# Performance work log

Measured on AMD Instinct MI355X. Metric: run time of the kernel, lower is better.

## Reference

```python
import jax, jax.numpy as jnp
import numpy as np

# Loihi neuron / simulation constants (params['neuron'], params['simulation'])
VTH_MANT = 80
V_DECAY = 128
I_DECAY = 1024
REF_DELAY = 1
WGT_EXP = 0
TAU_RHO = 1.0
SCALE_RHO = 1.0
TS = 1
THETA = float(VTH_MANT * (1 << 6))      # 5120, Loihi threshold in fixed-point units
W_SCALE = float(1 << (6 + WGT_EXP))     # 64, weight scaling into Loihi fixed point


def st_floor(x):
    """floor with straight-through gradient (Loihi integer truncation)."""
    return x + jax.lax.stop_gradient(jnp.floor(x) - x)


@jax.custom_vjp
def spike_fn(v):
    # binary spike scaled by 1/Ts, as in SLAYER-Loihi
    return (v >= THETA).astype(v.dtype) * (1.0 / TS)

def _spike_fwd(v):
    return spike_fn(v), v

def _spike_bwd(v, g):
    # SLAYER surrogate: scaleRho/(tauRho*theta) * exp(-|v - theta| / (tauRho*theta))
    pdf = (SCALE_RHO / (TAU_RHO * THETA)) * jnp.exp(-jnp.abs(v - THETA) / (TAU_RHO * THETA))
    return (g * pdf,)

spike_fn.defvjp(_spike_fwd, _spike_bwd)


def quantize_w(w, step=2.0):
    """SLAYER snn.utils.quantize(w, 2) with straight-through gradient."""
    return w + jax.lax.stop_gradient(jnp.round(w / step) * step - w)


def loihi_spikes(wsp):
    """Loihi CUBA neuron scan. wsp: [T, B, C] weighted spike input -> [T, B, C] spikes."""
    i_mul = (4096.0 - I_DECAY) / 4096.0
    v_mul = (4096.0 - V_DECAY) / 4096.0

    def step(carry, x):
        I, V, ref = carry
        I = st_floor(I * i_mul) + W_SCALE * x
        V = st_floor(V * v_mul) + I
        V = jnp.where(ref > 0, jnp.zeros_like(V), V)   # refractory hold at 0
        s = spike_fn(V)
        V = V * (1.0 - s * TS)                          # reset to 0 on spike
        ref = jnp.where(s > 0, REF_DELAY - 1, jnp.maximum(ref - 1, 0))
        return (I, V, ref), s

    B, C = wsp.shape[1], wsp.shape[2]
    init = (jnp.zeros((B, C), wsp.dtype),
            jnp.zeros((B, C), wsp.dtype),
            jnp.zeros((B, C), jnp.int32))
    _, s = jax.lax.scan(step, init, wsp)
    return s


def delay_shift(x):
    """delayShift(x, 1): shift spikes one step forward in time. x: [T, B, C]."""
    return jnp.concatenate([jnp.zeros_like(x[:1]), x[:-1]], axis=0)


def setup_inputs() -> dict:
    key = jax.random.key(0)
    k1, k2, k3 = jax.random.split(key, 3)
    B, IN, HID, OUT, T = 32, 1024, 2048, 512, 256
    spike_input = (jax.random.uniform(k1, (B, IN, T)) < 0.05).astype(jnp.float32)
    W1 = jax.random.normal(k2, (HID, IN), jnp.float32) * 8.0
    W2 = jax.random.normal(k3, (OUT, HID), jnp.float32) * 8.0
    return {"spike_input": spike_input, "W1": W1, "W2": W2}


def reference(spike_input, W1, W2):
    # spike_input: [B, IN, T] binary spikes
    x = jnp.transpose(spike_input, (2, 0, 1))          # [T, B, IN]
    w1 = quantize_w(W1)
    w2 = quantize_w(W2)
    h = jnp.einsum('tbi,hi->tbh', x, w1)               # fc1 per timestep
    s1 = delay_shift(loihi_spikes(h))                  # spikeLoihi + delayShift(1)
    o = jnp.einsum('tbh,oh->tbo', s1, w2)              # fc2 per timestep
    s2 = delay_shift(loihi_spikes(o))
    return jnp.transpose(s2, (1, 2, 0))                # [B, OUT, T]
```

## Files before the change

### kernel.cpp

```cpp
#include <hip/hip_runtime.h>

typedef unsigned char u8;
typedef signed char i8;
typedef unsigned int u32;
typedef __attribute__((ext_vector_type(4))) int i32x4;

#define AS1 __attribute__((address_space(1)))
#define AS3 __attribute__((address_space(3)))

__device__ __forceinline__ void gload_lds16(const void* g, void* l) {
    __builtin_amdgcn_global_load_lds((const AS1 void*)g, (AS3 void*)l, 16, 0, 0);
}

__global__ void transpose_x_bt(const float* __restrict__ X, i8* __restrict__ Xb,
                               int B, int IN, int T) {
    __shared__ float tile[128][33];
    const int t0 = blockIdx.x * 32, i0 = blockIdx.y * 128, b = blockIdx.z;
    const int tx = threadIdx.x & 31, ty = threadIdx.x >> 5;
    const float* src = X + (size_t)b * IN * T;
#pragma unroll
    for (int r = 0; r < 16; ++r) {
        int i = ty + r * 8;
        tile[i][tx] = src[(size_t)(i0 + i) * T + t0 + tx];
    }
    __syncthreads();
    const int cx = threadIdx.x & 31;
    const int tl0 = threadIdx.x >> 5;
#pragma unroll
    for (int r = 0; r < 4; ++r) {
        int tl = tl0 + r * 8;
        uchar4 pk;
        pk.x = (tile[cx * 4 + 0][tl] != 0.f) ? 1 : 0;
        pk.y = (tile[cx * 4 + 1][tl] != 0.f) ? 1 : 0;
        pk.z = (tile[cx * 4 + 2][tl] != 0.f) ? 1 : 0;
        pk.w = (tile[cx * 4 + 3][tl] != 0.f) ? 1 : 0;
        *(uchar4*)&Xb[((size_t)b * T + t0 + tl) * IN + i0 + cx * 4] = pk;
    }
}

__global__ void quant_both(const float4* __restrict__ W1, const float4* __restrict__ W2,
                           char4* __restrict__ W1q, char4* __restrict__ W2q,
                           int n1v, int n2v) {
    int i = blockIdx.x * 256 + threadIdx.x;
    if (i < n1v) {
        float4 w = W1[i];
        char4 q;
        q.x = (i8)(int)rintf(w.x * 0.5f);
        q.y = (i8)(int)rintf(w.y * 0.5f);
        q.z = (i8)(int)rintf(w.z * 0.5f);
        q.w = (i8)(int)rintf(w.w * 0.5f);
        W1q[i] = q;
    } else if (i < n1v + n2v) {
        int j = i - n1v;
        float4 w = W2[j];
        char4 q;
        q.x = (i8)(int)rintf(w.x * 0.5f);
        q.y = (i8)(int)rintf(w.y * 0.5f);
        q.z = (i8)(int)rintf(w.z * 0.5f);
        q.w = (i8)(int)rintf(w.w * 0.5f);
        W2q[j] = q;
    }
}

__global__ __launch_bounds__(256, 4) void gemm1_scan1(
        const i8* __restrict__ A, const i8* __restrict__ Bt,
        i8* __restrict__ S1, int K) {
    __shared__ __align__(16) i8 lds[40960];
    i8*    lA   = lds;
    i8*    lB   = lds + 32768;
    short* hT   = (short*)lds;
    u32*   bits = (u32*)(lds + 32768);

    const int nwg = gridDim.x;
    const int cpx = nwg >> 3;
    const int wg  = (blockIdx.x & 7) * cpx + (blockIdx.x >> 3);
    const int scanw = (blockIdx.x >> 3) & 3;
    const int bx = wg & 31;
    const int by = wg >> 5;
    const int n0 = bx * 64;
    const int m0 = by * 256;

    const int tid  = threadIdx.x;
    const int lane = tid & 63;
    const int w    = tid >> 6;
    const int l15 = lane & 15;
    const int l4  = lane >> 4;
    const int sw  = l15 & 7;

    i32x4 acc[4][4] = {};
    const int flatT = tid * 16;

    for (int k0 = 0; k0 < K; k0 += 128) {
        __syncthreads();
#pragma unroll
        for (int q = 0; q < 8; ++q) {
            int fl = q * 4096 + flatT;
            int r  = fl >> 7;
            int sc = ((fl >> 4) & 7) ^ (r & 7);
            gload_lds16(A + (size_t)(m0 + r) * K + k0 + sc * 16, &lA[fl]);
        }
#pragma unroll
        for (int q = 0; q < 2; ++q) {
            int fl = q * 4096 + flatT;
            int r  = fl >> 7;
            int sc = ((fl >> 4) & 7) ^ (r & 7);
            gload_lds16(Bt + (size_t)(n0 + r) * K + k0 + sc * 16, &lB[fl]);
        }
        __syncthreads();
#pragma unroll
        for (int kk = 0; kk < 2; ++kk) {
            i32x4 af[4], bf[4];
#pragma unroll
            for (int mf = 0; mf < 4; ++mf)
                af[mf] = *(const i32x4*)&lA[(w * 64 + mf * 16 + l15) * 128 +
                                            ((kk * 4 + l4) ^ sw) * 16];
#pragma unroll
            for (int nf = 0; nf < 4; ++nf)
                bf[nf] = *(const i32x4*)&lB[(nf * 16 + l15) * 128 +
                                            ((kk * 4 + l4) ^ sw) * 16];
#pragma unroll
            for (int mf = 0; mf < 4; ++mf)
#pragma unroll
                for (int nf = 0; nf < 4; ++nf)
                    acc[mf][nf] = __builtin_amdgcn_mfma_i32_16x16x64_i8(
                        af[mf], bf[nf], acc[mf][nf], 0, 0, 0);
        }
    }
    __syncthreads();

#pragma unroll
    for (int mf = 0; mf < 4; ++mf)
#pragma unroll
        for (int nf = 0; nf < 4; ++nf) {
            int n = nf * 16 + l15;
            int c = w * 16 + mf * 4 + l4;
            int h0 = acc[mf][nf][0] * 2, h1 = acc[mf][nf][1] * 2;
            int h2 = acc[mf][nf][2] * 2, h3 = acc[mf][nf][3] * 2;
            int2 pk;
            pk.x = (h0 & 0xffff) | (h1 << 16);
            pk.y = (h2 & 0xffff) | (h3 << 16);
            *(int2*)((char*)hT + n * 512 + ((c ^ (n & 15)) << 3)) = pk;
        }
    __syncthreads();

    if (w == scanw) {
        const int n = lane;
        const int nx = n & 15;
        const char* hrow = (char*)hT + n * 512;
        int2 ra[4], rb[4];
#pragma unroll
        for (int q = 0; q < 4; ++q)
            ra[q] = *(const int2*)(hrow + ((q ^ nx) << 3));
        u32 bw[8] = {0, 0, 0, 0, 0, 0, 0, 0};
        float I = 0.f, V = 0.f;
#pragma unroll
        for (int p = 0; p < 16; ++p) {
            if (p < 15) {
#pragma unroll
                for (int q = 0; q < 4; ++q) {
                    int2 v = *(const int2*)(hrow + ((((p + 1) * 4 + q) ^ nx) << 3));
                    if (p & 1) ra[q] = v; else rb[q] = v;
                }
            }
#pragma unroll
            for (int q = 0; q < 4; ++q) {
                int2 hh = (p & 1) ? rb[q] : ra[q];
#pragma unroll
                for (int j = 0; j < 4; ++j) {
                    int t = p * 16 + q * 4 + j;
                    short hv = (j == 0) ? (short)hh.x
                             : (j == 1) ? (short)(hh.x >> 16)
                             : (j == 2) ? (short)hh.y
                                        : (short)(hh.y >> 16);
                    I = floorf(I * 0.75f) + 64.f * (float)hv;
                    V = floorf(V * 0.96875f) + I;
                    if (V >= 5120.f) { bw[t >> 5] |= (1u << (t & 31)); V = 0.f; }
                }
            }
        }
#pragma unroll
        for (int wi = 0; wi < 8; ++wi) bits[wi * 64 + n] = bw[wi];
    }
    __syncthreads();

#pragma unroll
    for (int rep = 0; rep < 16; ++rep) {
        int d   = rep * 256 + tid;
        int tt  = d >> 4;
        int ndq = d & 15;
        u32 outw = 0;
        if (tt > 0) {
            int tb = tt - 1, wi = tb >> 5, sh = tb & 31;
            outw =  ((bits[wi * 64 + ndq * 4 + 0] >> sh) & 1)
                 | (((bits[wi * 64 + ndq * 4 + 1] >> sh) & 1) << 8)
                 | (((bits[wi * 64 + ndq * 4 + 2] >> sh) & 1) << 16)
                 | (((bits[wi * 64 + ndq * 4 + 3] >> sh) & 1) << 24);
        }
        *(u32*)&S1[(size_t)(m0 + tt) * 2048 + n0 + ndq * 4] = outw;
    }
}

__global__ __launch_bounds__(256, 1) void gemm2_scan2(
        const i8* __restrict__ A, const i8* __restrict__ Bt,
        float* __restrict__ out, int K) {
    __shared__ __align__(16) i8 lds[67584];
    i8*    lA   = lds;
    i8*    lB   = lds + 32768;
    float* hT   = (float*)lds;
    u32*   bits = (u32*)(lds + 65536);

    const int nwg = gridDim.x;
    const int cpx = nwg >> 3;
    const int wg  = (blockIdx.x & 7) * cpx + (blockIdx.x >> 3);
    const int scanw = (blockIdx.x >> 3) & 3;
    const int ox = wg & 7;
    const int by = wg >> 3;
    const int n0 = ox * 64;
    const int m0 = by * 256;

    const int tid  = threadIdx.x;
    const int lane = tid & 63;
    const int w    = tid >> 6;
    const int l15 = lane & 15;
    const int l4  = lane >> 4;
    const int sw  = l15 & 7;

    i32x4 acc[4][4] = {};
    const int flatT = tid * 16;

    for (int k0 = 0; k0 < K; k0 += 128) {
        __syncthreads();
#pragma unroll
        for (int q = 0; q < 8; ++q) {
            int fl = q * 4096 + flatT;
            int r  = fl >> 7;
            int sc = ((fl >> 4) & 7) ^ (r & 7);
            gload_lds16(A + (size_t)(m0 + r) * K + k0 + sc * 16, &lA[fl]);
        }
#pragma unroll
        for (int q = 0; q < 2; ++q) {
            int fl = q * 4096 + flatT;
            int r  = fl >> 7;
            int sc = ((fl >> 4) & 7) ^ (r & 7);
            gload_lds16(Bt + (size_t)(n0 + r) * K + k0 + sc * 16, &lB[fl]);
        }
        __syncthreads();
#pragma unroll
        for (int kk = 0; kk < 2; ++kk) {
            i32x4 af[4], bf[4];
#pragma unroll
            for (int mf = 0; mf < 4; ++mf)
                af[mf] = *(const i32x4*)&lA[(w * 64 + mf * 16 + l15) * 128 +
                                            ((kk * 4 + l4) ^ sw) * 16];
#pragma unroll
            for (int nf = 0; nf < 4; ++nf)
                bf[nf] = *(const i32x4*)&lB[(nf * 16 + l15) * 128 +
                                            ((kk * 4 + l4) ^ sw) * 16];
#pragma unroll
            for (int mf = 0; mf < 4; ++mf)
#pragma unroll
                for (int nf = 0; nf < 4; ++nf)
                    acc[mf][nf] = __builtin_amdgcn_mfma_i32_16x16x64_i8(
                        af[mf], bf[nf], acc[mf][nf], 0, 0, 0);
        }
    }
    __syncthreads();

#pragma unroll
    for (int mf = 0; mf < 4; ++mf)
#pragma unroll
        for (int nf = 0; nf < 4; ++nf) {
            int n = nf * 16 + l15;
            int c = w * 16 + mf * 4 + l4;
            float4 pk;
            pk.x = (float)(acc[mf][nf][0] * 2);
            pk.y = (float)(acc[mf][nf][1] * 2);
            pk.z = (float)(acc[mf][nf][2] * 2);
            pk.w = (float)(acc[mf][nf][3] * 2);
            *(float4*)((char*)hT + n * 1024 + ((c ^ (n & 15)) << 4)) = pk;
        }
    __syncthreads();

    if (w == scanw) {
        const int n = lane;
        const int nx = n & 15;
        const char* hrow = (char*)hT + n * 1024;
        float4 ra[4], rb[4];
#pragma unroll
        for (int q = 0; q < 4; ++q)
            ra[q] = *(const float4*)(hrow + ((q ^ nx) << 4));
        u32 bw[8] = {0, 0, 0, 0, 0, 0, 0, 0};
        float I = 0.f, V = 0.f;
#pragma unroll
        for (int p = 0; p < 16; ++p) {
            if (p < 15) {
#pragma unroll
                for (int q = 0; q < 4; ++q) {
                    float4 v = *(const float4*)(hrow + ((((p + 1) * 4 + q) ^ nx) << 4));
                    if (p & 1) ra[q] = v; else rb[q] = v;
                }
            }
#pragma unroll
            for (int q = 0; q < 4; ++q) {
                float4 hh = (p & 1) ? rb[q] : ra[q];
#pragma unroll
                for (int j = 0; j < 4; ++j) {
                    int t = p * 16 + q * 4 + j;
                    float hv = (j == 0) ? hh.x : (j == 1) ? hh.y
                             : (j == 2) ? hh.z : hh.w;
                    I = floorf(I * 0.75f) + 64.f * hv;
                    V = floorf(V * 0.96875f) + I;
                    if (V >= 5120.f) { bw[t >> 5] |= (1u << (t & 31)); V = 0.f; }
                }
            }
        }
#pragma unroll
        for (int wi = 0; wi < 8; ++wi) bits[wi * 64 + n] = bw[wi];
    }
    __syncthreads();

#pragma unroll
    for (int rep = 0; rep < 16; ++rep) {
        int flat = rep * 256 + tid;
        int o  = flat >> 6;
        int t4 = flat & 63;
        float4 v;
#pragma unroll
        for (int j = 0; j < 4; ++j) {
            int tt = t4 * 4 + j;
            float s = 0.f;
            if (tt > 0) {
                int tb = tt - 1;
                s = (float)((bits[(tb >> 5) * 64 + o] >> (tb & 31)) & 1);
            }
            if (j == 0) v.x = s; else if (j == 1) v.y = s;
            else if (j == 2) v.z = s; else v.w = s;
        }
        *(float4*)&out[((size_t)by * 512 + n0 + o) * 256 + t4 * 4] = v;
    }
}

extern "C" void kernel_launch(void* const* d_in, const int* in_sizes, int n_in,
                              void* d_out, int out_size, void* d_ws, size_t ws_size,
                              hipStream_t stream) {
    const int B = 32, IN = 1024, HID = 2048, OUT = 512, T = 256;
    const float* spikes = (const float*)d_in[0];
    const float* W1 = (const float*)d_in[1];
    const float* W2 = (const float*)d_in[2];
    float* out = (float*)d_out;

    char* ws = (char*)d_ws;
    size_t off = 0;
    auto alloc = [&](size_t bytes) -> void* {
        void* p = ws + off;
        off += (bytes + 255) & ~(size_t)255;
        return p;
    };
    i8* Xb  = (i8*)alloc((size_t)B * T * IN);
    i8* W1q = (i8*)alloc((size_t)HID * IN);
    i8* W2q = (i8*)alloc((size_t)OUT * HID);
    i8* S1  = (i8*)alloc((size_t)B * T * HID);

    dim3 blk(256);
    transpose_x_bt<<<dim3(T / 32, IN / 128, B), blk, 0, stream>>>(spikes, Xb, B, IN, T);
    {
        int n1v = HID * IN / 4, n2v = OUT * HID / 4;
        quant_both<<<dim3((n1v + n2v + 255) / 256), blk, 0, stream>>>(
            (const float4*)W1, (const float4*)W2, (char4*)W1q, (char4*)W2q, n1v, n2v);
    }
    gemm1_scan1<<<dim3(1024), blk, 0, stream>>>(Xb, W1q, S1, IN);
    gemm2_scan2<<<dim3(256), blk, 0, stream>>>(S1, W2q, out, HID);
}
```

Baseline: 75.47 us.

## Use 1024-thread blocks with double-buffered LDS pipeline in gemm2_scan2

gemm2_scan2 now runs 16 waves per workgroup instead of 4. Each wave owns a 16-row slice of the 256-row M tile rather than 64 rows. The K loop is double-buffered: the next 128-wide K tile is staged into the alternate LDS buffer while MFMA runs on the current one, leaving one barrier per iteration. The goal is more latency hiding and overlap of loads with compute, at the cost of higher LDS use (84 KB), less register reuse of B fragments per wave, and a serial per-block scan that now sits beside more idle waves.

```diff
diff --git a/kernel.cpp b/kernel.cpp
--- a/kernel.cpp
+++ b/kernel.cpp
@@ -200,19 +200,17 @@
     }
 }
 
-__global__ __launch_bounds__(256, 1) void gemm2_scan2(
+__global__ __launch_bounds__(1024, 1) void gemm2_scan2(
         const i8* __restrict__ A, const i8* __restrict__ Bt,
         float* __restrict__ out, int K) {
-    __shared__ __align__(16) i8 lds[67584];
-    i8*    lA   = lds;
-    i8*    lB   = lds + 32768;
+    __shared__ __align__(16) i8 lds[83968];
     float* hT   = (float*)lds;
-    u32*   bits = (u32*)(lds + 65536);
+    u32*   bits = (u32*)(lds + 81920);
 
     const int nwg = gridDim.x;
     const int cpx = nwg >> 3;
     const int wg  = (blockIdx.x & 7) * cpx + (blockIdx.x >> 3);
-    const int scanw = (blockIdx.x >> 3) & 3;
+    const int scanw = (blockIdx.x >> 3) & 15;
     const int ox = wg & 7;
     const int by = wg >> 3;
     const int n0 = ox * 64;
@@ -225,60 +223,66 @@
     const int l4  = lane >> 4;
     const int sw  = l15 & 7;
 
-    i32x4 acc[4][4] = {};
+    i32x4 acc[4] = {};
     const int flatT = tid * 16;
 
-    for (int k0 = 0; k0 < K; k0 += 128) {
-        __syncthreads();
-#pragma unroll
-        for (int q = 0; q < 8; ++q) {
-            int fl = q * 4096 + flatT;
+    auto STAGE = [&](int buf, int k0) {
+        i8* lA = lds + buf * 40960;
+        i8* lB = lA + 32768;
+#pragma unroll
+        for (int q = 0; q < 2; ++q) {
+            int fl = q * 16384 + flatT;
             int r  = fl >> 7;
             int sc = ((fl >> 4) & 7) ^ (r & 7);
             gload_lds16(A + (size_t)(m0 + r) * K + k0 + sc * 16, &lA[fl]);
         }
-#pragma unroll
-        for (int q = 0; q < 2; ++q) {
-            int fl = q * 4096 + flatT;
+        if (tid < 512) {
+            int fl = flatT;
             int r  = fl >> 7;
             int sc = ((fl >> 4) & 7) ^ (r & 7);
             gload_lds16(Bt + (size_t)(n0 + r) * K + k0 + sc * 16, &lB[fl]);
         }
-        __syncthreads();
+    };
+
+    auto COMPUTE = [&](int buf) {
+        const i8* lA = lds + buf * 40960;
+        const i8* lB = lA + 32768;
 #pragma unroll
         for (int kk = 0; kk < 2; ++kk) {
-            i32x4 af[4], bf[4];
-#pragma unroll
-            for (int mf = 0; mf < 4; ++mf)
-                af[mf] = *(const i32x4*)&lA[(w * 64 + mf * 16 + l15) * 128 +
-                                            ((kk * 4 + l4) ^ sw) * 16];
+            i32x4 af, bf[4];
+            af = *(const i32x4*)&lA[(w * 16 + l15) * 128 + ((kk * 4 + l4) ^ sw) * 16];
 #pragma unroll
             for (int nf = 0; nf < 4; ++nf)
                 bf[nf] = *(const i32x4*)&lB[(nf * 16 + l15) * 128 +
                                             ((kk * 4 + l4) ^ sw) * 16];
 #pragma unroll
-            for (int mf = 0; mf < 4; ++mf)
-#pragma unroll
-                for (int nf = 0; nf < 4; ++nf)
-                    acc[mf][nf] = __builtin_amdgcn_mfma_i32_16x16x64_i8(
-                        af[mf], bf[nf], acc[mf][nf], 0, 0, 0);
-        }
-    }
-    __syncthreads();
-
-#pragma unroll
-    for (int mf = 0; mf < 4; ++mf)
-#pragma unroll
-        for (int nf = 0; nf < 4; ++nf) {
-            int n = nf * 16 + l15;
-            int c = w * 16 + mf * 4 + l4;
-            float4 pk;
-            pk.x = (float)(acc[mf][nf][0] * 2);
-            pk.y = (float)(acc[mf][nf][1] * 2);
-            pk.z = (float)(acc[mf][nf][2] * 2);
-            pk.w = (float)(acc[mf][nf][3] * 2);
-            *(float4*)((char*)hT + n * 1024 + ((c ^ (n & 15)) << 4)) = pk;
-        }
+            for (int nf = 0; nf < 4; ++nf)
+                acc[nf] = __builtin_amdgcn_mfma_i32_16x16x64_i8(
+                    af, bf[nf], acc[nf], 0, 0, 0);
+        }
+    };
+
+    STAGE(0, 0);
+    __syncthreads();
+    int cur = 0;
+    for (int k0 = 0; k0 < K; k0 += 128) {
+        if (k0 + 128 < K) STAGE(cur ^ 1, k0 + 128);
+        COMPUTE(cur);
+        __syncthreads();
+        cur ^= 1;
+    }
+
+#pragma unroll
+    for (int nf = 0; nf < 4; ++nf) {
+        int n = nf * 16 + l15;
+        int c = w * 4 + l4;
+        float4 pk;
+        pk.x = (float)(acc[nf][0] * 2);
+        pk.y = (float)(acc[nf][1] * 2);
+        pk.z = (float)(acc[nf][2] * 2);
+        pk.w = (float)(acc[nf][3] * 2);
+        *(float4*)((char*)hT + n * 1024 + ((c ^ (n & 15)) << 4)) = pk;
+    }
     __syncthreads();
 
     if (w == scanw) {
@@ -320,8 +324,8 @@
     __syncthreads();
 
 #pragma unroll
-    for (int rep = 0; rep < 16; ++rep) {
-        int flat = rep * 256 + tid;
+    for (int rep = 0; rep < 4; ++rep) {
+        int flat = rep * 1024 + tid;
         int o  = flat >> 6;
         int t4 = flat & 63;
         float4 v;
@@ -361,13 +365,12 @@
     i8* W2q = (i8*)alloc((size_t)OUT * HID);
     i8* S1  = (i8*)alloc((size_t)B * T * HID);
 
-    dim3 blk(256);
-    transpose_x_bt<<<dim3(T / 32, IN / 128, B), blk, 0, stream>>>(spikes, Xb, B, IN, T);
+    transpose_x_bt<<<dim3(T / 32, IN / 128, B), dim3(256), 0, stream>>>(spikes, Xb, B, IN, T);
     {
         int n1v = HID * IN / 4, n2v = OUT * HID / 4;
-        quant_both<<<dim3((n1v + n2v + 255) / 256), blk, 0, stream>>>(
+        quant_both<<<dim3((n1v + n2v + 255) / 256), dim3(256), 0, stream>>>(
             (const float4*)W1, (const float4*)W2, (char4*)W1q, (char4*)W2q, n1v, n2v);
     }
-    gemm1_scan1<<<dim3(1024), blk, 0, stream>>>(Xb, W1q, S1, IN);
-    gemm2_scan2<<<dim3(256), blk, 0, stream>>>(S1, W2q, out, HID);
-}
+    gemm1_scan1<<<dim3(1024), dim3(256), 0, stream>>>(Xb, W1q, S1, IN);
+    gemm2_scan2<<<dim3(256), dim3(1024), 0, stream>>>(S1, W2q, out, HID);
+}
```

After: 68.13 us. 9.7% less time.
